# Optimization experiments

Hardware: AMD Instinct MI355X
Metric: run time of the kernel (lower is better)

The kernel has to match this reference:

```python
import jax, jax.numpy as jnp
import numpy as np

NHEADS = 16

def _unskew(X):
    # X: (B, M, M+L) -> (B, M, L); out[b,i,j] = X[b,i,i+j]
    B, M, T = X.shape
    L = T - M
    rows = jnp.arange(M)[:, None]            # (M,1)
    cols = rows + jnp.arange(L)[None, :]     # (M,L), values in [0, M+L-2]
    return X[:, rows, cols]

def _skew(X):
    # X: (B, M, L) -> (B, M, M+L), zero pad; out[b,i,i+j] = X[b,i,j]
    B, M, L = X.shape
    rows = jnp.arange(M)[:, None]
    cols = rows + jnp.arange(L)[None, :]
    out = jnp.zeros((B, M, M + L), dtype=X.dtype)
    return out.at[:, rows, cols].set(X)

def _heads(x, W, K):
    # x: (B,T,H) @ W^T -> (B,T,H) -> (B*K, T, D)
    y = x @ W.T
    B, T, H = y.shape
    D = H // K
    return y.reshape(B, T, K, D).transpose(0, 2, 1, 3).reshape(B * K, T, D)

def setup_inputs() -> dict:
    key = jax.random.key(0)
    ks = jax.random.split(key, 8)
    B, M, L, H = 8, 512, 1024, 1024
    D = H // NHEADS
    w = lambda k: jax.random.normal(k, (H, H), dtype=jnp.float32) * 0.02
    return {
        "query": jax.random.normal(ks[0], (B, M, H), dtype=jnp.float32),
        "key": jax.random.normal(ks[1], (B, M + L, H), dtype=jnp.float32),
        "value": jax.random.normal(ks[2], (B, M + L, H), dtype=jnp.float32),
        "key_pe": jax.random.normal(ks[3], (1, D, L), dtype=jnp.float32) * 0.02,
        "Wq": w(ks[4]),
        "Wk": w(ks[5]),
        "Wv": w(ks[6]),
        "Wo": w(ks[7]),
    }

def reference(query, key, value, key_pe, Wq, Wk, Wv, Wo):
    B, M, H = query.shape
    K = NHEADS
    D = H // K
    q = _heads(query, Wq, K)   # (BK, M, D)
    k = _heads(key, Wk, K)     # (BK, M+L, D)
    v = _heads(value, Wv, K)   # (BK, M+L, D)
    attn_cont = _unskew(jnp.einsum('bmd,btd->bmt', q, k))      # (BK, M, L)
    attn_pos = jnp.einsum('bmd,odl->bml', q, key_pe)            # (BK, M, L)
    attn = (attn_cont + attn_pos) / jnp.sqrt(jnp.asarray(D, q.dtype))
    attn = jax.nn.softmax(attn, axis=-1)
    out = jnp.einsum('bmt,btd->bmd', _skew(attn), v)            # (BK, M, D)
    out = out.reshape(B, K, M, D).transpose(0, 2, 1, 3).reshape(B, M, K * D)
    return out @ Wo.T
```

## Files before the change

kernel.cpp:

```cpp
#include <hip/hip_runtime.h>

using u16 = unsigned short;
using u32 = unsigned int;

typedef short bf16x8 __attribute__((ext_vector_type(8)));
typedef float f32x4 __attribute__((ext_vector_type(4)));
typedef float f32x16 __attribute__((ext_vector_type(16)));
typedef u16 u16x4 __attribute__((ext_vector_type(4)));
typedef u16 u16x8 __attribute__((ext_vector_type(8)));

__device__ __forceinline__ u16 f2b(float f) {
  u32 u = __builtin_bit_cast(u32, f);
  u += 0x7fffu + ((u >> 16) & 1u);
  return (u16)(u >> 16);
}
__device__ __forceinline__ u16 f2b_fast(float f) {
  u32 u = __builtin_bit_cast(u32, f);
  return (u16)((u + 0x8000u) >> 16);
}
__device__ __forceinline__ float b2f(u16 h) {
  u32 u = ((u32)h) << 16;
  return __builtin_bit_cast(float, u);
}
__device__ __forceinline__ f32x16 zero16() {
  f32x16 v;
#pragma unroll
  for (int i = 0; i < 16; ++i) v[i] = 0.f;
  return v;
}

typedef __attribute__((address_space(1))) const u16 gas_u16;
typedef __attribute__((address_space(3))) u16 las_u16;

__device__ __forceinline__ void gload16(const u16* g, u16* l) {
  __builtin_amdgcn_global_load_lds((const gas_u16*)g, (las_u16*)l, 16, 0, 0);
}

#define MFMA16(a, b, c) __builtin_amdgcn_mfma_f32_16x16x32_bf16((a), (b), (c), 0, 0, 0)
#define MFMA32(a, b, c) __builtin_amdgcn_mfma_f32_32x32x16_bf16((a), (b), (c), 0, 0, 0)

#define LOG2E 1.4426950408889634f


__global__ void k_cast_wpe(const float* __restrict__ Wq, const float* __restrict__ Wk,
                           const float* __restrict__ Wv, const float* __restrict__ Wo,
                           const float* __restrict__ pe, u16* __restrict__ wbf,
                           u16* __restrict__ pet) {
  const int bx = blockIdx.x;
  if (bx < 2048) {
    int i = bx * 256 + threadIdx.x;
    int wsel = i >> 17;
    int j = (i & 131071) * 8;
    const float* src = wsel == 0 ? Wq : wsel == 1 ? Wk : wsel == 2 ? Wv : Wo;
    float s = wsel == 0 ? 0.125f * LOG2E : 1.0f;
    f32x4 a = *(const f32x4*)(src + j);
    f32x4 b = *(const f32x4*)(src + j + 4);
    u16x8 o;
    o[0] = f2b(a[0] * s); o[1] = f2b(a[1] * s); o[2] = f2b(a[2] * s); o[3] = f2b(a[3] * s);
    o[4] = f2b(b[0] * s); o[5] = f2b(b[1] * s); o[6] = f2b(b[2] * s); o[7] = f2b(b[3] * s);
    *(u16x8*)(wbf + (size_t)wsel * 1048576 + j) = o;
  } else {
    int i = (bx - 2048) * 256 + threadIdx.x;
    int j = i >> 6, d = i & 63;
    pet[i] = f2b(pe[d * 1024 + j]);
  }
}


__global__ __launch_bounds__(256, 2) void k_proj(const float* __restrict__ query,
                                                 const float* __restrict__ key,
                                                 const float* __restrict__ value,
                                                 const u16* __restrict__ wbf,
                                                 u16* __restrict__ qb,
                                                 u16* __restrict__ kb,
                                                 u16* __restrict__ vtb) {
  __shared__ __align__(16) u16 As[128 * 32];
  __shared__ __align__(16) u16 Bs[128 * 32];
  const int tid = threadIdx.x;
  const int lane = tid & 63;
  const int w = tid >> 6;
  const int lr = lane & 15;
  const int lg = lane >> 4;
  const int wr = w >> 1;
  const int wc = w & 1;

  const int bx = blockIdx.x;
  int seg, lbx, segsz;
  const float* X;
  const u16* W;
  if (bx < 256)       { seg = 1; lbx = bx;        segsz = 256; X = query; W = wbf; }
  else if (bx < 1024) { seg = 2; lbx = bx - 256;  segsz = 768; X = key;   W = wbf + 1048576; }
  else                { seg = 3; lbx = bx - 1024; segsz = 768; X = value; W = wbf + 2097152; }
  const int bxs = (lbx & 7) * (segsz >> 3) + (lbx >> 3);
  const int c0 = (bxs & 7) << 7;
  const int r0 = (bxs >> 3) << 7;

  f32x4 acc[4][4];
#pragma unroll
  for (int i = 0; i < 4; ++i)
#pragma unroll
    for (int j = 0; j < 4; ++j) acc[i][j] = (f32x4){0.f, 0.f, 0.f, 0.f};

  const int srow = lane >> 2;
  const int sch = (lane & 3) * 8;
  const float* gA = X + (size_t)(r0 + w * 32 + srow) * 1024 + sch;
  const u16* gB = W + (size_t)(c0 + w * 32 + srow) * 1024 + sch;
  u16* lA = As + w * 32 * 32;
  u16* lB = Bs + w * 32 * 32;

  for (int kt = 0; kt < 32; ++kt) {
    const int k0 = kt * 32;
    f32x4 a0 = *(const f32x4*)(gA + k0);
    f32x4 a1 = *(const f32x4*)(gA + k0 + 4);
    f32x4 a2 = *(const f32x4*)(gA + k0 + 16 * 1024);
    f32x4 a3 = *(const f32x4*)(gA + k0 + 16 * 1024 + 4);
    u16x8 p0, p1;
    p0[0] = f2b(a0[0]); p0[1] = f2b(a0[1]); p0[2] = f2b(a0[2]); p0[3] = f2b(a0[3]);
    p0[4] = f2b(a1[0]); p0[5] = f2b(a1[1]); p0[6] = f2b(a1[2]); p0[7] = f2b(a1[3]);
    p1[0] = f2b(a2[0]); p1[1] = f2b(a2[1]); p1[2] = f2b(a2[2]); p1[3] = f2b(a2[3]);
    p1[4] = f2b(a3[0]); p1[5] = f2b(a3[1]); p1[6] = f2b(a3[2]); p1[7] = f2b(a3[3]);
    *(u16x8*)(lA + srow * 32 + sch) = p0;
    *(u16x8*)(lA + (16 + srow) * 32 + sch) = p1;
    gload16(gB + k0, lB);
    gload16(gB + k0 + 16 * 1024, lB + 16 * 32);
    __syncthreads();
    bf16x8 af[4], bfr[4];
#pragma unroll
    for (int mi = 0; mi < 4; ++mi)
      af[mi] = *(const bf16x8*)(As + (wr * 64 + mi * 16 + lr) * 32 + lg * 8);
#pragma unroll
    for (int ci = 0; ci < 4; ++ci)
      bfr[ci] = *(const bf16x8*)(Bs + (wc * 64 + ci * 16 + lr) * 32 + lg * 8);
#pragma unroll
    for (int mi = 0; mi < 4; ++mi)
#pragma unroll
      for (int ci = 0; ci < 4; ++ci) acc[mi][ci] = MFMA16(af[mi], bfr[ci], acc[mi][ci]);
    __syncthreads();
  }

  const int rbase = r0 + wr * 64;
  const int cbase = c0 + wc * 64;
  if (seg == 1) {
#pragma unroll
    for (int mi = 0; mi < 4; ++mi)
#pragma unroll
      for (int ci = 0; ci < 4; ++ci) {
        const int c = cbase + ci * 16 + lr;
        const int h = c >> 6, d = c & 63;
        const int rr = rbase + mi * 16 + lg * 4;
#pragma unroll
        for (int r = 0; r < 4; ++r) {
          const int rg = rr + r;
          const int b = rg >> 9, mm = rg & 511;
          qb[((size_t)(b * 16 + h) * 512 + mm) * 64 + d] = f2b(acc[mi][ci][r]);
        }
      }
  } else if (seg == 2) {
#pragma unroll
    for (int mi = 0; mi < 4; ++mi)
#pragma unroll
      for (int ci = 0; ci < 4; ++ci) {
        const int c = cbase + ci * 16 + lr;
        const int h = c >> 6, d = c & 63;
        const int rr = rbase + mi * 16 + lg * 4;
#pragma unroll
        for (int r = 0; r < 4; ++r) {
          const int rg = rr + r;
          const int b = rg / 1536;
          const int t = rg - b * 1536;
          kb[((size_t)(b * 16 + h) * 1536 + t) * 64 + d] = f2b(acc[mi][ci][r]);
        }
      }
  } else {
#pragma unroll
    for (int mi = 0; mi < 4; ++mi)
#pragma unroll
      for (int ci = 0; ci < 4; ++ci) {
        const int c = cbase + ci * 16 + lr;
        const int h = c >> 6, d = c & 63;
        const int rr = rbase + mi * 16 + lg * 4;
        const int b = rr / 1536;
        const int t = rr - b * 1536;
        u16x4 pk;
#pragma unroll
        for (int r = 0; r < 4; ++r) pk[r] = f2b(acc[mi][ci][r]);
        *(u16x4*)(vtb + ((size_t)(b * 16 + h) * 64 + d) * 1536 + t) = pk;
      }
  }
}


__global__ __launch_bounds__(256, 2) void k_out(const u16* __restrict__ X,
                                                const u16* __restrict__ W,
                                                float* __restrict__ Y) {
  __shared__ __align__(16) u16 As[128 * 32];
  __shared__ __align__(16) u16 Bs[128 * 32];
  const int tid = threadIdx.x;
  const int lane = tid & 63;
  const int w = tid >> 6;
  const int lr = lane & 15;
  const int lg = lane >> 4;
  const int wr = w >> 1;
  const int wc = w & 1;
  const int bx = blockIdx.x;
  const int bxs = (bx & 7) * 32 + (bx >> 3);
  const int c0 = (bxs & 7) << 7;
  const int r0 = (bxs >> 3) << 7;

  f32x4 acc[4][4];
#pragma unroll
  for (int i = 0; i < 4; ++i)
#pragma unroll
    for (int j = 0; j < 4; ++j) acc[i][j] = (f32x4){0.f, 0.f, 0.f, 0.f};

  const int srow = lane >> 2;
  const int sch = (lane & 3) * 8;
  const u16* gA = X + (size_t)(r0 + w * 32 + srow) * 1024 + sch;
  const u16* gB = W + (size_t)(c0 + w * 32 + srow) * 1024 + sch;
  u16* lA = As + w * 32 * 32;
  u16* lB = Bs + w * 32 * 32;

  for (int kt = 0; kt < 32; ++kt) {
    const int k0 = kt * 32;
    gload16(gA + k0, lA);
    gload16(gA + k0 + 16 * 1024, lA + 16 * 32);
    gload16(gB + k0, lB);
    gload16(gB + k0 + 16 * 1024, lB + 16 * 32);
    __syncthreads();
    bf16x8 af[4], bfr[4];
#pragma unroll
    for (int mi = 0; mi < 4; ++mi)
      af[mi] = *(const bf16x8*)(As + (wr * 64 + mi * 16 + lr) * 32 + lg * 8);
#pragma unroll
    for (int ci = 0; ci < 4; ++ci)
      bfr[ci] = *(const bf16x8*)(Bs + (wc * 64 + ci * 16 + lr) * 32 + lg * 8);
#pragma unroll
    for (int mi = 0; mi < 4; ++mi)
#pragma unroll
      for (int ci = 0; ci < 4; ++ci) acc[mi][ci] = MFMA16(af[mi], bfr[ci], acc[mi][ci]);
    __syncthreads();
  }

  const int rbase = r0 + wr * 64;
  const int cbase = c0 + wc * 64;
#pragma unroll
  for (int mi = 0; mi < 4; ++mi)
#pragma unroll
    for (int ci = 0; ci < 4; ++ci) {
      const int c = cbase + ci * 16 + lr;
      const int rr = rbase + mi * 16 + lg * 4;
#pragma unroll
      for (int r = 0; r < 4; ++r) Y[(size_t)(rr + r) * 1024 + c] = acc[mi][ci][r];
    }
}


__global__ __launch_bounds__(256, 2) void k_attn(const u16* __restrict__ qb,
                                                 const u16* __restrict__ kb,
                                                 const u16* __restrict__ vtb,
                                                 const u16* __restrict__ pet,
                                                 u16* __restrict__ ctx) {
  __shared__ __align__(16) u16 posk[32 * 1060];
  __shared__ __align__(16) u16 Pb[4][32 * 40];

  const int tid = threadIdx.x;
  const int lane = tid & 63;
  const int w = tid >> 6;
  const int ml = lane & 31;
  const int hi = lane >> 5;
  const int bx = blockIdx.x;
  const int swz = (bx & 7) * 256 + (bx >> 3);
  const int bk = swz >> 4;
  const int m0 = (swz & 15) << 5;

  const u16* Qh = qb + (size_t)bk * (512 * 64);
  const u16* Kh = kb + (size_t)bk * (1536 * 64);
  const u16* Vh = vtb + (size_t)bk * (64 * 1536);

  bf16x8 qf[4];
#pragma unroll
  for (int ks = 0; ks < 4; ++ks)
    qf[ks] = *(const bf16x8*)(Qh + (m0 + ml) * 64 + ks * 16 + hi * 8);

  for (int jt = 0; jt < 8; ++jt) {
    const int j0 = w * 256 + jt * 32;
    f32x16 c = zero16();
#pragma unroll
    for (int ks = 0; ks < 4; ++ks) {
      bf16x8 a = *(const bf16x8*)(pet + (j0 + ml) * 64 + ks * 16 + hi * 8);
      c = MFMA32(a, qf[ks], c);
    }
#pragma unroll
    for (int r = 0; r < 16; ++r) {
      const int tl = (r & 3) + 8 * (r >> 2) + 4 * hi;
      posk[ml * 1060 + j0 + tl + ml] = f2b_fast(c[r]);
    }
  }
  __syncthreads();

  float mrun = -1e30f, lrun = 0.f;
  f32x16 oA = zero16(), oB = zero16();

  auto loadKV = [&](bf16x8(&kf)[4], bf16x8(&vf)[2][2], int s) {
    const int t0 = m0 + s * 32;
#pragma unroll
    for (int ks = 0; ks < 4; ++ks)
      kf[ks] = *(const bf16x8*)(Kh + (t0 + ml) * 64 + ks * 16 + hi * 8);
#pragma unroll
    for (int dt = 0; dt < 2; ++dt)
#pragma unroll
      for (int kt = 0; kt < 2; ++kt)
        vf[dt][kt] = *(const bf16x8*)(Vh + (dt * 32 + ml) * 1536 + t0 + kt * 16 + hi * 8);
  };

  auto doTile = [&](int s, bf16x8(&kf)[4], bf16x8(&vf)[2][2]) {
    __builtin_amdgcn_s_setprio(1);
    f32x16 sc = zero16();
#pragma unroll
    for (int ks = 0; ks < 4; ++ks) sc = MFMA32(kf[ks], qf[ks], sc);
    __builtin_amdgcn_s_setprio(0);

    const bool edge = (s == 0) | (s == 32);
#pragma unroll
    for (int q = 0; q < 4; ++q) {
      const u16x4 pk = *(const u16x4*)(posk + ml * 1060 + s * 32 + q * 8 + hi * 4);
#pragma unroll
      for (int r0 = 0; r0 < 4; ++r0) {
        const int r = q * 4 + r0;
        float v = sc[r] + b2f(pk[r0]);
        if (edge) {
          const int j = s * 32 + q * 8 + hi * 4 + r0 - ml;
          v = (j >= 0 && j < 1024) ? v : -1e30f;
        }
        sc[r] = v;
      }
    }

    float a0 = fmaxf(fmaxf(sc[0], sc[1]), fmaxf(sc[2], sc[3]));
    float a1 = fmaxf(fmaxf(sc[4], sc[5]), fmaxf(sc[6], sc[7]));
    float a2 = fmaxf(fmaxf(sc[8], sc[9]), fmaxf(sc[10], sc[11]));
    float a3 = fmaxf(fmaxf(sc[12], sc[13]), fmaxf(sc[14], sc[15]));
    float pmax = fmaxf(fmaxf(a0, a1), fmaxf(a2, a3));
    pmax = fmaxf(pmax, __shfl_xor(pmax, 32));

    if (__ballot(pmax > mrun)) {
      const float mn = fmaxf(mrun, pmax);
      const float scale = __builtin_amdgcn_exp2f(mrun - mn);
      lrun *= scale;
      mrun = mn;
#pragma unroll
      for (int r = 0; r < 16; ++r) { oA[r] *= scale; oB[r] *= scale; }
    }

#pragma unroll
    for (int r = 0; r < 16; ++r) sc[r] = __builtin_amdgcn_exp2f(sc[r] - mrun);
    float s0 = (sc[0] + sc[1]) + (sc[2] + sc[3]);
    float s1 = (sc[4] + sc[5]) + (sc[6] + sc[7]);
    float s2 = (sc[8] + sc[9]) + (sc[10] + sc[11]);
    float s3 = (sc[12] + sc[13]) + (sc[14] + sc[15]);
    float rs = (s0 + s1) + (s2 + s3);
    rs += __shfl_xor(rs, 32);
    lrun += rs;

#pragma unroll
    for (int q = 0; q < 4; ++q) {
      u16x4 pk;
#pragma unroll
      for (int r0 = 0; r0 < 4; ++r0) pk[r0] = f2b_fast(sc[q * 4 + r0]);
      *(u16x4*)(&Pb[w][ml * 40 + q * 8 + hi * 4]) = pk;
    }
    asm volatile("" ::: "memory");
    bf16x8 pb0 = *(const bf16x8*)(&Pb[w][ml * 40 + hi * 8]);
    bf16x8 pb1 = *(const bf16x8*)(&Pb[w][ml * 40 + 16 + hi * 8]);

    __builtin_amdgcn_s_setprio(1);
    oA = MFMA32(vf[0][0], pb0, oA);
    oB = MFMA32(vf[1][0], pb0, oB);
    oA = MFMA32(vf[0][1], pb1, oA);
    oB = MFMA32(vf[1][1], pb1, oB);
    __builtin_amdgcn_s_setprio(0);
  };

  bf16x8 kfA[4], kfB[4], vfA[2][2], vfB[2][2];
  loadKV(kfA, vfA, w);
  for (int s = w;;) {
    const int sn = s + 4;
    if (sn <= 32) loadKV(kfB, vfB, sn);
    doTile(s, kfA, vfA);
    if (sn > 32) break;
    s = sn;
    const int sn2 = s + 4;
    if (sn2 <= 32) loadKV(kfA, vfA, sn2);
    doTile(s, kfB, vfB);
    if (sn2 > 32) break;
    s = sn2;
  }

  __syncthreads();
  float* mO = (float*)posk;
  float* mM = mO + 4 * 32 * 68;
  float* mL = mM + 128;
#pragma unroll
  for (int q = 0; q < 4; ++q) {
    *(f32x4*)(mO + (w * 32 + ml) * 68 + q * 8 + hi * 4) =
        (f32x4){oA[4 * q], oA[4 * q + 1], oA[4 * q + 2], oA[4 * q + 3]};
    *(f32x4*)(mO + (w * 32 + ml) * 68 + 32 + q * 8 + hi * 4) =
        (f32x4){oB[4 * q], oB[4 * q + 1], oB[4 * q + 2], oB[4 * q + 3]};
  }
  if (hi == 0) {
    mM[w * 32 + ml] = mrun;
    mL[w * 32 + ml] = lrun;
  }
  __syncthreads();

  const int m = tid >> 3;
  const int d0 = (tid & 7) * 8;
  float mw4[4], lw4[4], M = -3e38f;
#pragma unroll
  for (int i = 0; i < 4; ++i) {
    mw4[i] = mM[i * 32 + m];
    lw4[i] = mL[i * 32 + m];
    M = fmaxf(M, mw4[i]);
  }
  float den = 0.f;
  float o[8] = {0.f, 0.f, 0.f, 0.f, 0.f, 0.f, 0.f, 0.f};
#pragma unroll
  for (int i = 0; i < 4; ++i) {
    const float e = __builtin_amdgcn_exp2f(mw4[i] - M);
    den += lw4[i] * e;
    f32x4 a = *(const f32x4*)(mO + (i * 32 + m) * 68 + d0);
    f32x4 b = *(const f32x4*)(mO + (i * 32 + m) * 68 + d0 + 4);
#pragma unroll
    for (int r = 0; r < 4; ++r) {
      o[r] += e * a[r];
      o[4 + r] += e * b[r];
    }
  }
  const float inv = 1.f / den;
  u16x8 ov;
#pragma unroll
  for (int i = 0; i < 8; ++i) ov[i] = f2b_fast(o[i] * inv);
  const int b_ = bk >> 4, h = bk & 15;
  *(u16x8*)(ctx + ((size_t)(b_ * 512 + m0 + m)) * 1024 + h * 64 + d0) = ov;
}


extern "C" void kernel_launch(void* const* d_in, const int* in_sizes, int n_in,
                              void* d_out, int out_size, void* d_ws, size_t ws_size,
                              hipStream_t stream) {
  (void)in_sizes; (void)n_in; (void)out_size; (void)ws_size;
  const float* query = (const float*)d_in[0];
  const float* key   = (const float*)d_in[1];
  const float* value = (const float*)d_in[2];
  const float* pe    = (const float*)d_in[3];
  const float* Wq    = (const float*)d_in[4];
  const float* Wk    = (const float*)d_in[5];
  const float* Wv    = (const float*)d_in[6];
  const float* Wo    = (const float*)d_in[7];

  u16* wbf = (u16*)d_ws;
  u16* pet = wbf + 4194304;
  u16* qb  = pet + 65536;
  u16* kb  = qb + 4194304;
  u16* vtb = kb + 12582912;
  u16* ctx = vtb + 12582912;

  k_cast_wpe<<<2304, 256, 0, stream>>>(Wq, Wk, Wv, Wo, pe, wbf, pet);
  k_proj<<<1792, 256, 0, stream>>>(query, key, value, wbf, qb, kb, vtb);
  k_attn<<<2048, 256, 0, stream>>>(qb, kb, vtb, pet, ctx);
  k_out<<<256, 256, 0, stream>>>(ctx, wbf + 3145728, (float*)d_out);
}
```

Measured before the change: 221.5 us.

## Double K-tile depth in projection GEMM with padded A and XOR-swizzled B LDS

```diff
diff --git a/kernel.cpp b/kernel.cpp
--- a/kernel.cpp
+++ b/kernel.cpp
@@ -74,8 +74,8 @@
                                                  u16* __restrict__ qb,
                                                  u16* __restrict__ kb,
                                                  u16* __restrict__ vtb) {
-  __shared__ __align__(16) u16 As[128 * 32];
-  __shared__ __align__(16) u16 Bs[128 * 32];
+  __shared__ __align__(16) u16 As[128 * 72];
+  __shared__ __align__(16) u16 Bs[128 * 64];
   const int tid = threadIdx.x;
   const int lane = tid & 63;
   const int w = tid >> 6;
@@ -101,40 +101,50 @@
 #pragma unroll
     for (int j = 0; j < 4; ++j) acc[i][j] = (f32x4){0.f, 0.f, 0.f, 0.f};
 
-  const int srow = lane >> 2;
-  const int sch = (lane & 3) * 8;
-  const float* gA = X + (size_t)(r0 + w * 32 + srow) * 1024 + sch;
-  const u16* gB = W + (size_t)(c0 + w * 32 + srow) * 1024 + sch;
-  u16* lA = As + w * 32 * 32;
-  u16* lB = Bs + w * 32 * 32;
-
-  for (int kt = 0; kt < 32; ++kt) {
-    const int k0 = kt * 32;
-    f32x4 a0 = *(const f32x4*)(gA + k0);
-    f32x4 a1 = *(const f32x4*)(gA + k0 + 4);
-    f32x4 a2 = *(const f32x4*)(gA + k0 + 16 * 1024);
-    f32x4 a3 = *(const f32x4*)(gA + k0 + 16 * 1024 + 4);
-    u16x8 p0, p1;
-    p0[0] = f2b(a0[0]); p0[1] = f2b(a0[1]); p0[2] = f2b(a0[2]); p0[3] = f2b(a0[3]);
-    p0[4] = f2b(a1[0]); p0[5] = f2b(a1[1]); p0[6] = f2b(a1[2]); p0[7] = f2b(a1[3]);
-    p1[0] = f2b(a2[0]); p1[1] = f2b(a2[1]); p1[2] = f2b(a2[2]); p1[3] = f2b(a2[3]);
-    p1[4] = f2b(a3[0]); p1[5] = f2b(a3[1]); p1[6] = f2b(a3[2]); p1[7] = f2b(a3[3]);
-    *(u16x8*)(lA + srow * 32 + sch) = p0;
-    *(u16x8*)(lA + (16 + srow) * 32 + sch) = p1;
-    gload16(gB + k0, lB);
-    gload16(gB + k0 + 16 * 1024, lB + 16 * 32);
+  const int arow = tid >> 1;
+  const int acol = (tid & 1) * 32;
+  const float* gA = X + (size_t)(r0 + arow) * 1024 + acol;
+  const int brow_off = lane >> 3;
+  const int bslot = (lane & 7) ^ (lane >> 3);
+  u16* lB = Bs + w * 32 * 64;
+
+  for (int kt = 0; kt < 16; ++kt) {
+    const int k0 = kt * 64;
+#pragma unroll
+    for (int c = 0; c < 4; ++c) {
+      const u16* g = W + (size_t)(c0 + w * 32 + c * 8 + brow_off) * 1024 + k0 + bslot * 8;
+      gload16(g, lB + c * 8 * 64);
+    }
+    f32x4 av[8];
+#pragma unroll
+    for (int i = 0; i < 8; ++i) av[i] = *(const f32x4*)(gA + k0 + i * 4);
+#pragma unroll
+    for (int ch = 0; ch < 4; ++ch) {
+      u16x8 p;
+#pragma unroll
+      for (int e = 0; e < 8; ++e) p[e] = f2b(av[ch * 2 + (e >> 2)][e & 3]);
+      *(u16x8*)(As + arow * 72 + acol + ch * 8) = p;
+    }
     __syncthreads();
-    bf16x8 af[4], bfr[4];
-#pragma unroll
-    for (int mi = 0; mi < 4; ++mi)
-      af[mi] = *(const bf16x8*)(As + (wr * 64 + mi * 16 + lr) * 32 + lg * 8);
-#pragma unroll
-    for (int ci = 0; ci < 4; ++ci)
-      bfr[ci] = *(const bf16x8*)(Bs + (wc * 64 + ci * 16 + lr) * 32 + lg * 8);
-#pragma unroll
-    for (int mi = 0; mi < 4; ++mi)
-#pragma unroll
-      for (int ci = 0; ci < 4; ++ci) acc[mi][ci] = MFMA16(af[mi], bfr[ci], acc[mi][ci]);
+    bf16x8 af[2][4], bfr[2][4];
+#pragma unroll
+    for (int kk = 0; kk < 2; ++kk) {
+#pragma unroll
+      for (int mi = 0; mi < 4; ++mi)
+        af[kk][mi] = *(const bf16x8*)(As + (wr * 64 + mi * 16 + lr) * 72 + kk * 32 + lg * 8);
+#pragma unroll
+      for (int ci = 0; ci < 4; ++ci) {
+        const int row = wc * 64 + ci * 16 + lr;
+        bfr[kk][ci] = *(const bf16x8*)(Bs + row * 64 + (((kk * 4 + lg) ^ (row & 7)) * 8));
+      }
+    }
+#pragma unroll
+    for (int kk = 0; kk < 2; ++kk)
+#pragma unroll
+      for (int mi = 0; mi < 4; ++mi)
+#pragma unroll
+        for (int ci = 0; ci < 4; ++ci)
+          acc[mi][ci] = MFMA16(af[kk][mi], bfr[kk][ci], acc[mi][ci]);
     __syncthreads();
   }
 
```

After: 265.6 us. +19.9%, slower.

## Double-buffer projection GEMM LDS tiles and pad A rows

Applied to the files above, without the earlier changes.

```diff
diff --git a/kernel.cpp b/kernel.cpp
--- a/kernel.cpp
+++ b/kernel.cpp
@@ -67,15 +67,15 @@
 }
 
 
-__global__ __launch_bounds__(256, 2) void k_proj(const float* __restrict__ query,
+__global__ __launch_bounds__(256, 3) void k_proj(const float* __restrict__ query,
                                                  const float* __restrict__ key,
                                                  const float* __restrict__ value,
                                                  const u16* __restrict__ wbf,
                                                  u16* __restrict__ qb,
                                                  u16* __restrict__ kb,
                                                  u16* __restrict__ vtb) {
-  __shared__ __align__(16) u16 As[128 * 32];
-  __shared__ __align__(16) u16 Bs[128 * 32];
+  __shared__ __align__(16) u16 As[2][128 * 40];
+  __shared__ __align__(16) u16 Bs[2][128 * 32];
   const int tid = threadIdx.x;
   const int lane = tid & 63;
   const int w = tid >> 6;
@@ -105,37 +105,63 @@
   const int sch = (lane & 3) * 8;
   const float* gA = X + (size_t)(r0 + w * 32 + srow) * 1024 + sch;
   const u16* gB = W + (size_t)(c0 + w * 32 + srow) * 1024 + sch;
-  u16* lA = As + w * 32 * 32;
-  u16* lB = Bs + w * 32 * 32;
-
-  for (int kt = 0; kt < 32; ++kt) {
-    const int k0 = kt * 32;
-    f32x4 a0 = *(const f32x4*)(gA + k0);
-    f32x4 a1 = *(const f32x4*)(gA + k0 + 4);
-    f32x4 a2 = *(const f32x4*)(gA + k0 + 16 * 1024);
-    f32x4 a3 = *(const f32x4*)(gA + k0 + 16 * 1024 + 4);
+  const int aoff = (w * 32 + srow) * 40 + sch;
+  const int boff = w * 1024;
+
+  {
+    f32x4 a0 = *(const f32x4*)(gA);
+    f32x4 a1 = *(const f32x4*)(gA + 4);
+    f32x4 a2 = *(const f32x4*)(gA + 16 * 1024);
+    f32x4 a3 = *(const f32x4*)(gA + 16 * 1024 + 4);
+    gload16(gB, &Bs[0][boff]);
+    gload16(gB + 16 * 1024, &Bs[0][boff + 16 * 32]);
     u16x8 p0, p1;
     p0[0] = f2b(a0[0]); p0[1] = f2b(a0[1]); p0[2] = f2b(a0[2]); p0[3] = f2b(a0[3]);
     p0[4] = f2b(a1[0]); p0[5] = f2b(a1[1]); p0[6] = f2b(a1[2]); p0[7] = f2b(a1[3]);
     p1[0] = f2b(a2[0]); p1[1] = f2b(a2[1]); p1[2] = f2b(a2[2]); p1[3] = f2b(a2[3]);
     p1[4] = f2b(a3[0]); p1[5] = f2b(a3[1]); p1[6] = f2b(a3[2]); p1[7] = f2b(a3[3]);
-    *(u16x8*)(lA + srow * 32 + sch) = p0;
-    *(u16x8*)(lA + (16 + srow) * 32 + sch) = p1;
-    gload16(gB + k0, lB);
-    gload16(gB + k0 + 16 * 1024, lB + 16 * 32);
+    *(u16x8*)(&As[0][aoff]) = p0;
+    *(u16x8*)(&As[0][aoff + 16 * 40]) = p1;
+  }
+
+  for (int kt = 0; kt < 32; ++kt) {
+    const int cur = kt & 1;
+    const int nxt = cur ^ 1;
     __syncthreads();
+
+    f32x4 n0, n1, n2, n3;
+    const bool more = (kt < 31);
+    if (more) {
+      const int k1 = (kt + 1) * 32;
+      n0 = *(const f32x4*)(gA + k1);
+      n1 = *(const f32x4*)(gA + k1 + 4);
+      n2 = *(const f32x4*)(gA + k1 + 16 * 1024);
+      n3 = *(const f32x4*)(gA + k1 + 16 * 1024 + 4);
+      gload16(gB + k1, &Bs[nxt][boff]);
+      gload16(gB + k1 + 16 * 1024, &Bs[nxt][boff + 16 * 32]);
+    }
+
     bf16x8 af[4], bfr[4];
 #pragma unroll
     for (int mi = 0; mi < 4; ++mi)
-      af[mi] = *(const bf16x8*)(As + (wr * 64 + mi * 16 + lr) * 32 + lg * 8);
+      af[mi] = *(const bf16x8*)(&As[cur][(wr * 64 + mi * 16 + lr) * 40 + lg * 8]);
 #pragma unroll
     for (int ci = 0; ci < 4; ++ci)
-      bfr[ci] = *(const bf16x8*)(Bs + (wc * 64 + ci * 16 + lr) * 32 + lg * 8);
+      bfr[ci] = *(const bf16x8*)(&Bs[cur][(wc * 64 + ci * 16 + lr) * 32 + lg * 8]);
 #pragma unroll
     for (int mi = 0; mi < 4; ++mi)
 #pragma unroll
       for (int ci = 0; ci < 4; ++ci) acc[mi][ci] = MFMA16(af[mi], bfr[ci], acc[mi][ci]);
-    __syncthreads();
+
+    if (more) {
+      u16x8 p0, p1;
+      p0[0] = f2b(n0[0]); p0[1] = f2b(n0[1]); p0[2] = f2b(n0[2]); p0[3] = f2b(n0[3]);
+      p0[4] = f2b(n1[0]); p0[5] = f2b(n1[1]); p0[6] = f2b(n1[2]); p0[7] = f2b(n1[3]);
+      p1[0] = f2b(n2[0]); p1[1] = f2b(n2[1]); p1[2] = f2b(n2[2]); p1[3] = f2b(n2[3]);
+      p1[4] = f2b(n3[0]); p1[5] = f2b(n3[1]); p1[6] = f2b(n3[2]); p1[7] = f2b(n3[3]);
+      *(u16x8*)(&As[nxt][aoff]) = p0;
+      *(u16x8*)(&As[nxt][aoff + 16 * 40]) = p1;
+    }
   }
 
   const int rbase = r0 + wr * 64;
```

New measurement: 220.4 us. About the same (-0.5%).
